# Kernel optimization log

Measured on AMD Instinct MI355X. Metric: run time of the kernel, lower is better.

The kernel has to match this reference:

```python
import jax, jax.numpy as jnp
import numpy as np

N_NODES = 100000


def _graph_conv(x, W, b, src, dst, n_nodes):
    # dgl GraphConv, norm='both'. in_dim >= out_dim so weight is applied first.
    E = src.shape[0]
    ones = jnp.ones((E,), dtype=x.dtype)
    deg_out = jnp.clip(jax.ops.segment_sum(ones, src, num_segments=n_nodes), 1.0)
    deg_in = jnp.clip(jax.ops.segment_sum(ones, dst, num_segments=n_nodes), 1.0)
    h = x @ W                                  # [N, out]
    h = h * (deg_out ** -0.5)[:, None]          # src-side norm D_out^{-1/2}
    agg = jax.ops.segment_sum(h[src], dst, num_segments=n_nodes)  # SpMM
    agg = agg * (deg_in ** -0.5)[:, None]       # dst-side norm D_in^{-1/2}
    return agg + b


def setup_inputs() -> dict:
    key = jax.random.key(0)
    k1, k2, k3, k4, k5, k6, k7 = jax.random.split(key, 7)
    in_dim, hidden_dim, out_dim = 256, 128, 40
    E = 3200000
    h = jax.random.normal(k1, (N_NODES, in_dim), dtype=jnp.float32)
    src = jax.random.randint(k2, (E,), 0, N_NODES)
    dst = jax.random.randint(k3, (E,), 0, N_NODES)
    # Glorot-style init for GraphConv weights, zero bias (dgl default)
    W1 = jax.random.normal(k4, (in_dim, hidden_dim), dtype=jnp.float32) / np.sqrt(in_dim)
    b1 = jnp.zeros((hidden_dim,), dtype=jnp.float32)
    W2 = jax.random.normal(k5, (hidden_dim, out_dim), dtype=jnp.float32) / np.sqrt(hidden_dim)
    b2 = jnp.zeros((out_dim,), dtype=jnp.float32)
    return {"h": h, "W1": W1, "b1": b1, "W2": W2, "b2": b2, "src": src, "dst": dst}


def reference(h, W1, b1, W2, b2, src, dst):
    n = h.shape[0]
    # CRD: GraphConv -> relu (dropout is identity in eval)
    x = _graph_conv(h, W1, b1, src, dst, n)
    x = jax.nn.relu(x)
    # CLS: GraphConv -> log_softmax over classes
    x = _graph_conv(x, W2, b2, src, dst, n)
    return jax.nn.log_softmax(x, axis=1)
```

## Files before the change

kernel.cpp:

```cpp
#include <hip/hip_runtime.h>
#include <hip/hip_bf16.h>
#include <cstddef>
#include <cstdint>

#define IN_DIM 256
#define HID 128
#define OUT_DIM 40

#define CHUNK 8192
#define BIN_SHIFT 10
#define BIN_SIZE 1024
#define MAXB 128
#define GSPLIT 8

typedef __attribute__((ext_vector_type(8))) short short8;
typedef __attribute__((ext_vector_type(4))) float f32x4;
typedef __attribute__((ext_vector_type(2))) float f32x2;

__device__ inline short f2bf(float f) {
    __hip_bfloat16 b = __float2bfloat16(f);
    return __builtin_bit_cast(short, b);
}
__device__ inline float bf2f(unsigned short u) {
    unsigned int v = (unsigned int)u << 16;
    return __builtin_bit_cast(float, v);
}
__device__ inline int permf(int p) { return (p >> 3) + 16 * (p & 7); }

__global__ __launch_bounds__(256) void k_binscatter(const int* __restrict__ src, const int* __restrict__ dst,
                                                    uint32_t* __restrict__ stD, unsigned short* __restrict__ stS,
                                                    int* __restrict__ bboD, int* __restrict__ bboS,
                                                    int E, int NBINS) {
    __shared__ int hD[MAXB], hS[MAXB], cD[MAXB], cS[MAXB], sd[MAXB];
    int j = blockIdx.x, t = threadIdx.x;
    int base = j * CHUNK;
    int nE = min(CHUNK, E - base);
    int NB1 = NBINS + 1;
    for (int i = t; i < MAXB; i += 256) { hD[i] = 0; hS[i] = 0; }
    __syncthreads();
    for (int i = t; i < nE; i += 256) {
        atomicAdd(&hD[dst[base + i] >> BIN_SHIFT], 1);
        atomicAdd(&hS[src[base + i] >> BIN_SHIFT], 1);
    }
    __syncthreads();
    if (t < MAXB) sd[t] = hD[t];
    __syncthreads();
    for (int off = 1; off < MAXB; off <<= 1) {
        int x = 0;
        if (t < MAXB && t >= off) x = sd[t - off];
        __syncthreads();
        if (t < MAXB) sd[t] += x;
        __syncthreads();
    }
    if (t < MAXB) cD[t] = sd[t] - hD[t];
    if (t < NBINS) bboD[(size_t)j * NB1 + t] = sd[t] - hD[t];
    if (t == NBINS) bboD[(size_t)j * NB1 + NBINS] = nE;
    __syncthreads();
    if (t < MAXB) sd[t] = hS[t];
    __syncthreads();
    for (int off = 1; off < MAXB; off <<= 1) {
        int x = 0;
        if (t < MAXB && t >= off) x = sd[t - off];
        __syncthreads();
        if (t < MAXB) sd[t] += x;
        __syncthreads();
    }
    if (t < MAXB) cS[t] = sd[t] - hS[t];
    if (t < NBINS) bboS[(size_t)j * NB1 + t] = sd[t] - hS[t];
    if (t == NBINS) bboS[(size_t)j * NB1 + NBINS] = nE;
    __syncthreads();
    for (int i = t; i < nE; i += 256) {
        int s = src[base + i], d = dst[base + i];
        int pD = atomicAdd(&cD[d >> BIN_SHIFT], 1);
        stD[(size_t)base + pD] = ((uint32_t)(d & (BIN_SIZE - 1)) << 17) | (uint32_t)s;
        int pS = atomicAdd(&cS[s >> BIN_SHIFT], 1);
        stS[(size_t)base + pS] = (unsigned short)(s & (BIN_SIZE - 1));
    }
}

__global__ __launch_bounds__(256) void k_deg_dst(const uint32_t* __restrict__ stD, const int* __restrict__ bboD,
                                                 int* __restrict__ deg_in, int* __restrict__ hsave,
                                                 int N, int nchunk, int NBINS) {
    __shared__ int hist[BIN_SIZE];
    int b = blockIdx.x, g = blockIdx.y, t = threadIdx.x;
    int wv = t >> 6, lane = t & 63;
    int NB1 = NBINS + 1;
    for (int i = t; i < BIN_SIZE; i += 256) hist[i] = 0;
    __syncthreads();
    for (int j = g * 4 + wv; j < nchunk; j += GSPLIT * 4) {
        int s = bboD[(size_t)j * NB1 + b], e = bboD[(size_t)j * NB1 + b + 1];
        const uint32_t* seg = stD + (size_t)j * CHUNK;
        for (int i = s + lane; i < e; i += 64)
            atomicAdd(&hist[seg[i] >> 17], 1);
    }
    __syncthreads();
    int base = b << BIN_SHIFT;
    int* hp = hsave + ((size_t)(b * GSPLIT + g) << BIN_SHIFT);
    for (int i = t; i < BIN_SIZE; i += 256) {
        int v = hist[i];
        hp[i] = v;
        if (v) atomicAdd(&deg_in[base + i], v);
    }
}

__global__ __launch_bounds__(256) void k_deg_src(const unsigned short* __restrict__ stS, const int* __restrict__ bboS,
                                                 int* __restrict__ deg_out, int N, int nchunk, int NBINS) {
    __shared__ int hist[BIN_SIZE];
    int b = blockIdx.x, g = blockIdx.y, t = threadIdx.x;
    int wv = t >> 6, lane = t & 63;
    int NB1 = NBINS + 1;
    for (int i = t; i < BIN_SIZE; i += 256) hist[i] = 0;
    __syncthreads();
    for (int j = g * 4 + wv; j < nchunk; j += GSPLIT * 4) {
        int s = bboS[(size_t)j * NB1 + b], e = bboS[(size_t)j * NB1 + b + 1];
        const unsigned short* seg = stS + (size_t)j * CHUNK;
        for (int i = s + lane; i < e; i += 64)
            atomicAdd(&hist[seg[i]], 1);
    }
    __syncthreads();
    int base = b << BIN_SHIFT;
    for (int i = t; i < BIN_SIZE; i += 256) {
        int v = hist[i];
        if (v) atomicAdd(&deg_out[base + i], v);
    }
}

__global__ __launch_bounds__(256) void k_col(const uint32_t* __restrict__ stD, const int* __restrict__ bboD,
                                             const int* __restrict__ hsave, int* __restrict__ cursor,
                                             int* __restrict__ col, int N, int nchunk, int NBINS) {
    __shared__ int hist[BIN_SIZE];
    int b = blockIdx.x, g = blockIdx.y, t = threadIdx.x;
    int wv = t >> 6, lane = t & 63;
    int NB1 = NBINS + 1;
    int base = b << BIN_SHIFT;
    const int* hp = hsave + ((size_t)(b * GSPLIT + g) << BIN_SHIFT);
    for (int i = t; i < BIN_SIZE; i += 256) {
        int v = hp[i];
        hist[i] = v ? atomicAdd(&cursor[base + i], v) : 0;
    }
    __syncthreads();
    for (int j = g * 4 + wv; j < nchunk; j += GSPLIT * 4) {
        int s = bboD[(size_t)j * NB1 + b], e = bboD[(size_t)j * NB1 + b + 1];
        const uint32_t* seg = stD + (size_t)j * CHUNK;
        for (int i = s + lane; i < e; i += 64) {
            uint32_t v = seg[i];
            int pos = atomicAdd(&hist[v >> 17], 1);
            col[pos] = (int)(v & 0x1FFFFu);
        }
    }
}

__global__ __launch_bounds__(256) void k_scan1(const int* __restrict__ deg, int* __restrict__ out,
                                               int* __restrict__ bsum, float* __restrict__ rs_in, int n) {
    __shared__ int sd[256];
    int t = threadIdx.x, b = blockIdx.x;
    int base = b * 1024 + t * 4;
    int v0 = 0, v1 = 0, v2 = 0, v3 = 0;
    if (base + 0 < n) v0 = deg[base + 0];
    if (base + 1 < n) v1 = deg[base + 1];
    if (base + 2 < n) v2 = deg[base + 2];
    if (base + 3 < n) v3 = deg[base + 3];
    if (base + 0 < n) rs_in[base + 0] = rsqrtf((float)max(v0, 1));
    if (base + 1 < n) rs_in[base + 1] = rsqrtf((float)max(v1, 1));
    if (base + 2 < n) rs_in[base + 2] = rsqrtf((float)max(v2, 1));
    if (base + 3 < n) rs_in[base + 3] = rsqrtf((float)max(v3, 1));
    int ts = v0 + v1 + v2 + v3;
    sd[t] = ts;
    __syncthreads();
    for (int off = 1; off < 256; off <<= 1) {
        int x = 0;
        if (t >= off) x = sd[t - off];
        __syncthreads();
        sd[t] += x;
        __syncthreads();
    }
    int excl = sd[t] - ts;
    if (base + 0 < n) out[base + 0] = excl;
    if (base + 1 < n) out[base + 1] = excl + v0;
    if (base + 2 < n) out[base + 2] = excl + v0 + v1;
    if (base + 3 < n) out[base + 3] = excl + v0 + v1 + v2;
    if (t == 255) bsum[b] = sd[255];
}

__global__ __launch_bounds__(1024) void k_scan2(int* __restrict__ bsum, int nb) {
    __shared__ int sd[1024];
    int t = threadIdx.x;
    int v = (t < nb) ? bsum[t] : 0;
    sd[t] = v;
    __syncthreads();
    for (int off = 1; off < 1024; off <<= 1) {
        int x = 0;
        if (t >= off) x = sd[t - off];
        __syncthreads();
        sd[t] += x;
        __syncthreads();
    }
    if (t < nb) bsum[t] = sd[t] - v;
}

__global__ __launch_bounds__(256) void k_scan3(int* __restrict__ row_ptr, const int* __restrict__ bsum,
                                               int* __restrict__ cursor, const int* __restrict__ deg_out,
                                               float* __restrict__ rs_out, int n, int E) {
    int i = blockIdx.x * 256 + threadIdx.x;
    if (i < n) {
        int v = row_ptr[i] + bsum[i >> 10];
        row_ptr[i] = v;
        cursor[i] = v;
        rs_out[i] = rsqrtf((float)max(deg_out[i], 1));
    }
    if (i == 0) row_ptr[n] = E;
}

__global__ __launch_bounds__(256) void k_wrepack(const float* __restrict__ B, short* __restrict__ Wg) {
    int u = blockIdx.x * 256 + threadIdx.x;
    int k = u >> 5;
    int n0 = (u & 31) * 4;
    float4 v = *(const float4*)(B + (size_t)k * HID + n0);
    int ks = k >> 5, quad = (k >> 3) & 3, j = k & 7;
    float vv[4] = {v.x, v.y, v.z, v.w};
#pragma unroll
    for (int e = 0; e < 4; ++e) {
        int n = n0 + e;
        int nt = n >> 4;
        int ln = (n & 15) | (quad << 4);
        Wg[(((nt * 8 + ks) * 64) + ln) * 8 + j] = f2bf(vv[e]);
    }
}

__global__ __launch_bounds__(256) void k_w2repack(const float* __restrict__ W2, const float* __restrict__ b1,
                                                  short* __restrict__ Wg2, float* __restrict__ b1p) {
    int t = blockIdx.x * 256 + threadIdx.x;
    if (t < 3 * 4 * 64 * 8) {
        int f = t >> 9;
        int ln = (t >> 3) & 63;
        int j = t & 7;
        int nt = f >> 2, ks = f & 3;
        int q = ks * 32 + (ln >> 4) * 8 + j;
        int c = nt * 16 + (ln & 15);
        float v = (c < OUT_DIM) ? W2[(size_t)permf(q) * OUT_DIM + c] : 0.f;
        Wg2[t] = f2bf(v);
    }
    if (t < HID) b1p[t] = b1[permf(t)];
}

__global__ __launch_bounds__(256) void k_gemm1(const float* __restrict__ A, const short* __restrict__ Wg,
                                               const float* __restrict__ rs_out, uint32_t* __restrict__ h1f, int M) {
    __shared__ short As[64 * 264];
    int t = threadIdx.x;
    int lane = t & 63, wv = t >> 6;
    int block_row = blockIdx.x * 64;
#pragma unroll
    for (int i = 0; i < 16; ++i) {
        int u = t + i * 256;
        int row = u >> 6, kq = (u & 63) * 4;
        int gr = block_row + row;
        float4 v = {0.f, 0.f, 0.f, 0.f};
        if (gr < M) v = *(const float4*)(A + (size_t)gr * IN_DIM + kq);
        short4 sv = {f2bf(v.x), f2bf(v.y), f2bf(v.z), f2bf(v.w)};
        *(short4*)&As[row * 264 + kq] = sv;
    }
    __syncthreads();
    f32x4 acc[8] = {};
    int arow = (wv * 16 + (lane & 15)) * 264 + (lane >> 4) * 8;
#pragma unroll
    for (int ks = 0; ks < 8; ++ks) {
        short8 a = *(short8*)&As[arow + ks * 32];
#pragma unroll
        for (int nt = 0; nt < 8; ++nt) {
            short8 b = *(const short8*)&Wg[(((nt * 8 + ks) * 64) + lane) * 8];
            acc[nt] = __builtin_amdgcn_mfma_f32_16x16x32_bf16(a, b, acc[nt], 0, 0, 0);
        }
    }
    int quad = lane >> 4, cl = lane & 15;
#pragma unroll
    for (int r = 0; r < 4; ++r) {
        int gr = block_row + wv * 16 + quad * 4 + r;
        if (gr >= M) continue;
        float sc = rs_out[gr];
        int d0 = __builtin_amdgcn_cvt_pk_fp8_f32(acc[0][r] * sc, acc[1][r] * sc, 0, false);
        d0 = __builtin_amdgcn_cvt_pk_fp8_f32(acc[2][r] * sc, acc[3][r] * sc, d0, true);
        int d1 = __builtin_amdgcn_cvt_pk_fp8_f32(acc[4][r] * sc, acc[5][r] * sc, 0, false);
        d1 = __builtin_amdgcn_cvt_pk_fp8_f32(acc[6][r] * sc, acc[7][r] * sc, d1, true);
        uint2 dd = make_uint2((uint32_t)d0, (uint32_t)d1);
        *(uint2*)((char*)h1f + (size_t)gr * 128 + cl * 8) = dd;
    }
}

__global__ __launch_bounds__(256) void k_spmm1f(const uint2* __restrict__ h1f2, const int* __restrict__ rp,
                                                const int* __restrict__ col, const float* __restrict__ rs_in,
                                                const float* __restrict__ rs_out, const float* __restrict__ b1p,
                                                const short* __restrict__ Wg2,
                                                unsigned char* __restrict__ h2f, int N) {
    __shared__ uint32_t x1s[16 * 64];
    __shared__ uint32_t hs[160];
    int t = threadIdx.x;
    int wv = t >> 6, lane = t & 63;
    int grp = lane >> 4, ql = lane & 15;
    int w_base = blockIdx.x * 16;

    int ntl = (wv < 3) ? wv : 0;
    short8 wf0 = *(const short8*)&Wg2[((ntl * 4 + 0) * 64 + lane) * 8];
    short8 wf1 = *(const short8*)&Wg2[((ntl * 4 + 1) * 64 + lane) * 8];
    short8 wf2 = *(const short8*)&Wg2[((ntl * 4 + 2) * 64 + lane) * 8];
    short8 wf3 = *(const short8*)&Wg2[((ntl * 4 + 3) * 64 + lane) * 8];
    float4 blo = *(const float4*)&b1p[ql * 8];
    float4 bhi = *(const float4*)&b1p[ql * 8 + 4];

    for (int i = t; i < 16 * 64; i += 256) x1s[i] = 0;
    __syncthreads();

#pragma unroll 1
    for (int q = 0; q < 4; ++q) {
        int nloc = wv * 4 + q;
        int w = w_base + nloc;
        if (w < N) {
            int s = rp[w], e = rp[w + 1];
            float acc[8] = {};
            int i = s;
            while (i < e) {
                int cnt = min(64, e - i);
                int cl = (lane < cnt) ? lane : cnt - 1;
                int cidx = col[i + cl];
                for (int it = 0; it < cnt; it += 8) {
                    int eA = it + grp, eB = it + 4 + grp;
                    int cA = __shfl(cidx, eA, 64);
                    int cB = __shfl(cidx, eB, 64);
                    float mA = (eA < cnt) ? 1.f : 0.f;
                    float mB = (eB < cnt) ? 1.f : 0.f;
                    uint2 uA = h1f2[(size_t)cA * 16 + ql];
                    uint2 uB = h1f2[(size_t)cB * 16 + ql];
                    {
                        f32x2 p0 = __builtin_amdgcn_cvt_pk_f32_fp8(uA.x, false);
                        f32x2 p1 = __builtin_amdgcn_cvt_pk_f32_fp8(uA.x, true);
                        f32x2 p2 = __builtin_amdgcn_cvt_pk_f32_fp8(uA.y, false);
                        f32x2 p3 = __builtin_amdgcn_cvt_pk_f32_fp8(uA.y, true);
                        acc[0] = fmaf(p0.x, mA, acc[0]); acc[1] = fmaf(p0.y, mA, acc[1]);
                        acc[2] = fmaf(p1.x, mA, acc[2]); acc[3] = fmaf(p1.y, mA, acc[3]);
                        acc[4] = fmaf(p2.x, mA, acc[4]); acc[5] = fmaf(p2.y, mA, acc[5]);
                        acc[6] = fmaf(p3.x, mA, acc[6]); acc[7] = fmaf(p3.y, mA, acc[7]);
                    }
                    {
                        f32x2 p0 = __builtin_amdgcn_cvt_pk_f32_fp8(uB.x, false);
                        f32x2 p1 = __builtin_amdgcn_cvt_pk_f32_fp8(uB.x, true);
                        f32x2 p2 = __builtin_amdgcn_cvt_pk_f32_fp8(uB.y, false);
                        f32x2 p3 = __builtin_amdgcn_cvt_pk_f32_fp8(uB.y, true);
                        acc[0] = fmaf(p0.x, mB, acc[0]); acc[1] = fmaf(p0.y, mB, acc[1]);
                        acc[2] = fmaf(p1.x, mB, acc[2]); acc[3] = fmaf(p1.y, mB, acc[3]);
                        acc[4] = fmaf(p2.x, mB, acc[4]); acc[5] = fmaf(p2.y, mB, acc[5]);
                        acc[6] = fmaf(p3.x, mB, acc[6]); acc[7] = fmaf(p3.y, mB, acc[7]);
                    }
                }
                i += cnt;
            }
#pragma unroll
            for (int j = 0; j < 8; ++j) {
                acc[j] += __shfl_xor(acc[j], 16, 64);
                acc[j] += __shfl_xor(acc[j], 32, 64);
            }
            if (lane < 16) {
                float sc = rs_in[w];
                float f0, f1;
                uint32_t o0, o1, o2, o3;
                f0 = fmaxf(fmaf(acc[0], sc, blo.x), 0.f); f1 = fmaxf(fmaf(acc[1], sc, blo.y), 0.f);
                o0 = (uint32_t)(unsigned short)f2bf(f0) | ((uint32_t)(unsigned short)f2bf(f1) << 16);
                f0 = fmaxf(fmaf(acc[2], sc, blo.z), 0.f); f1 = fmaxf(fmaf(acc[3], sc, blo.w), 0.f);
                o1 = (uint32_t)(unsigned short)f2bf(f0) | ((uint32_t)(unsigned short)f2bf(f1) << 16);
                f0 = fmaxf(fmaf(acc[4], sc, bhi.x), 0.f); f1 = fmaxf(fmaf(acc[5], sc, bhi.y), 0.f);
                o2 = (uint32_t)(unsigned short)f2bf(f0) | ((uint32_t)(unsigned short)f2bf(f1) << 16);
                f0 = fmaxf(fmaf(acc[6], sc, bhi.z), 0.f); f1 = fmaxf(fmaf(acc[7], sc, bhi.w), 0.f);
                o3 = (uint32_t)(unsigned short)f2bf(f0) | ((uint32_t)(unsigned short)f2bf(f1) << 16);
                int woff = (nloc * 256 + ql * 16) ^ ((nloc & 7) << 4);
                *(uint4*)((char*)x1s + woff) = make_uint4(o0, o1, o2, o3);
            }
        }
    }
    __syncthreads();
    int vr = min(16, N - w_base);
    if (wv < 3) {
        int row = lane & 15, kc = lane >> 4;
        int rbase = row * 256 + kc * 16;
        int swz = (row & 7) << 4;
        f32x4 c = {};
        c = __builtin_amdgcn_mfma_f32_16x16x32_bf16(*(short8*)((char*)x1s + ((rbase + 0) ^ swz)),   wf0, c, 0, 0, 0);
        c = __builtin_amdgcn_mfma_f32_16x16x32_bf16(*(short8*)((char*)x1s + ((rbase + 64) ^ swz)),  wf1, c, 0, 0, 0);
        c = __builtin_amdgcn_mfma_f32_16x16x32_bf16(*(short8*)((char*)x1s + ((rbase + 128) ^ swz)), wf2, c, 0, 0, 0);
        c = __builtin_amdgcn_mfma_f32_16x16x32_bf16(*(short8*)((char*)x1s + ((rbase + 192) ^ swz)), wf3, c, 0, 0, 0);
        int cc = wv * 16 + row;
        int r0 = kc * 4;
        if (cc < OUT_DIM) {
#pragma unroll
            for (int r = 0; r < 4; ++r) {
                int node = r0 + r;
                if (node < vr) {
                    float v = c[r] * rs_out[w_base + node];
                    int pk = __builtin_amdgcn_cvt_pk_fp8_f32(v, v, 0, false);
                    ((unsigned char*)hs)[node * 40 + cc] = (unsigned char)(pk & 0xff);
                }
            }
        }
    }
    __syncthreads();
    uint32_t* dp = (uint32_t*)(h2f + (size_t)w_base * 40);
    for (int idx = t; idx < vr * 10; idx += 256) dp[idx] = hs[idx];
}

__global__ __launch_bounds__(256) void k_spmm2(const unsigned char* __restrict__ h2f, const int* __restrict__ rp,
                                               const int* __restrict__ col, const float* __restrict__ rs_in,
                                               const float* __restrict__ b2, float* __restrict__ out, int n) {
    int w = (blockIdx.x * 256 + threadIdx.x) >> 6;
    int lane = threadIdx.x & 63;
    if (w >= n) return;
    int grp = lane / 5;
    int dw = lane - grp * 5;
    bool gval = grp < 12;
    int s = rp[w], e = rp[w + 1];
    float acc[8] = {};
    int i = s;
    while (i < e) {
        int cnt = min(64, e - i);
        int cl = (lane < cnt) ? lane : cnt - 1;
        int cidx = col[i + cl];
        for (int it = 0; it < cnt; it += 24) {
            int eA = it + grp, eB = it + 12 + grp;
            int cA = __shfl(cidx, eA & 63, 64);
            int cB = __shfl(cidx, eB & 63, 64);
            float mA = (gval && eA < cnt) ? 1.f : 0.f;
            float mB = (gval && eB < cnt) ? 1.f : 0.f;
            uint2 uA = *(const uint2*)(h2f + (size_t)cA * 40 + dw * 8);
            uint2 uB = *(const uint2*)(h2f + (size_t)cB * 40 + dw * 8);
            {
                f32x2 p0 = __builtin_amdgcn_cvt_pk_f32_fp8(uA.x, false);
                f32x2 p1 = __builtin_amdgcn_cvt_pk_f32_fp8(uA.x, true);
                f32x2 p2 = __builtin_amdgcn_cvt_pk_f32_fp8(uA.y, false);
                f32x2 p3 = __builtin_amdgcn_cvt_pk_f32_fp8(uA.y, true);
                acc[0] = fmaf(p0.x, mA, acc[0]); acc[1] = fmaf(p0.y, mA, acc[1]);
                acc[2] = fmaf(p1.x, mA, acc[2]); acc[3] = fmaf(p1.y, mA, acc[3]);
                acc[4] = fmaf(p2.x, mA, acc[4]); acc[5] = fmaf(p2.y, mA, acc[5]);
                acc[6] = fmaf(p3.x, mA, acc[6]); acc[7] = fmaf(p3.y, mA, acc[7]);
            }
            {
                f32x2 p0 = __builtin_amdgcn_cvt_pk_f32_fp8(uB.x, false);
                f32x2 p1 = __builtin_amdgcn_cvt_pk_f32_fp8(uB.x, true);
                f32x2 p2 = __builtin_amdgcn_cvt_pk_f32_fp8(uB.y, false);
                f32x2 p3 = __builtin_amdgcn_cvt_pk_f32_fp8(uB.y, true);
                acc[0] = fmaf(p0.x, mB, acc[0]); acc[1] = fmaf(p0.y, mB, acc[1]);
                acc[2] = fmaf(p1.x, mB, acc[2]); acc[3] = fmaf(p1.y, mB, acc[3]);
                acc[4] = fmaf(p2.x, mB, acc[4]); acc[5] = fmaf(p2.y, mB, acc[5]);
                acc[6] = fmaf(p3.x, mB, acc[6]); acc[7] = fmaf(p3.y, mB, acc[7]);
            }
        }
        i += cnt;
    }
#pragma unroll
    for (int j = 0; j < 8; ++j) {
        acc[j] += __shfl(acc[j], (lane + 30) & 63, 64);
        acc[j] += __shfl(acc[j], (lane + 15) & 63, 64);
        acc[j] += __shfl(acc[j], (lane + 5) & 63, 64) + __shfl(acc[j], (lane + 10) & 63, 64);
    }
    bool act = lane < 5;
    float sc = rs_in[w];
    float val[8];
#pragma unroll
    for (int j = 0; j < 8; ++j)
        val[j] = fmaf(acc[j], sc, b2[dw * 8 + j]);
    float pm = -INFINITY;
    if (act) {
        pm = val[0];
#pragma unroll
        for (int j = 1; j < 8; ++j) pm = fmaxf(pm, val[j]);
    }
    pm = fmaxf(pm, __shfl_xor(pm, 4, 8));
    pm = fmaxf(pm, __shfl_xor(pm, 2, 8));
    pm = fmaxf(pm, __shfl_xor(pm, 1, 8));
    float ex = 0.f;
    if (act) {
#pragma unroll
        for (int j = 0; j < 8; ++j) ex += expf(val[j] - pm);
    }
    ex += __shfl_xor(ex, 4, 8);
    ex += __shfl_xor(ex, 2, 8);
    ex += __shfl_xor(ex, 1, 8);
    if (act) {
        float l = pm + logf(ex);
        float4 o0 = {val[0] - l, val[1] - l, val[2] - l, val[3] - l};
        float4 o1 = {val[4] - l, val[5] - l, val[6] - l, val[7] - l};
        float* op = out + (size_t)w * OUT_DIM + dw * 8;
        *(float4*)op = o0;
        *(float4*)(op + 4) = o1;
    }
}


extern "C" void kernel_launch(void* const* d_in, const int* in_sizes, int n_in,
                              void* d_out, int out_size, void* d_ws, size_t ws_size,
                              hipStream_t stream) {
    const int N = in_sizes[0] / IN_DIM;
    const int E = in_sizes[5];
    const float* h  = (const float*)d_in[0];
    const float* W1 = (const float*)d_in[1];
    const float* b1 = (const float*)d_in[2];
    const float* W2 = (const float*)d_in[3];
    const float* b2 = (const float*)d_in[4];
    const int* src  = (const int*)d_in[5];
    const int* dst  = (const int*)d_in[6];
    float* out = (float*)d_out;

    const int NBINS  = (N + BIN_SIZE - 1) >> BIN_SHIFT;
    const int NCHUNK = (E + CHUNK - 1) / CHUNK;

    char* w = (char*)d_ws;
    size_t off = 0;
    auto alloc = [&](size_t bytes) -> void* {
        void* p = w + off;
        off += (bytes + 255) & ~(size_t)255;
        return p;
    };
    int* deg_in   = (int*)alloc((size_t)N * 4);
    int* deg_out  = (int*)alloc((size_t)N * 4);
    int* row_ptr  = (int*)alloc((size_t)(N + 1) * 4);
    int* cursor   = (int*)alloc((size_t)N * 4);
    int* bsum     = (int*)alloc(1024 * 4);
    float* rs_out = (float*)alloc((size_t)N * 4);
    float* rs_in  = (float*)alloc((size_t)N * 4);
    int* col      = (int*)alloc((size_t)E * 4);
    int* bboD     = (int*)alloc((size_t)NCHUNK * (NBINS + 1) * 4);
    int* bboS     = (int*)alloc((size_t)NCHUNK * (NBINS + 1) * 4);
    short* Wg     = (short*)alloc((size_t)8 * 8 * 64 * 8 * 2);
    short* Wg2    = (short*)alloc((size_t)3 * 4 * 64 * 8 * 2);
    float* b1p    = (float*)alloc((size_t)HID * 4);
    int* hsave    = (int*)alloc((size_t)NBINS * GSPLIT * BIN_SIZE * 4);
    size_t stD_bytes = (size_t)E * 4;  if ((size_t)N * HID > stD_bytes) stD_bytes = (size_t)N * HID;
    size_t stS_bytes = (size_t)E * 2;  if ((size_t)N * OUT_DIM > stS_bytes) stS_bytes = (size_t)N * OUT_DIM;
    uint32_t* stD = (uint32_t*)alloc(stD_bytes);
    unsigned short* stS = (unsigned short*)alloc(stS_bytes);
    uint32_t* h1f = (uint32_t*)stD;
    unsigned char* h2f = (unsigned char*)stS;

    int gN = (N + 255) / 256;
    int NB = (N + 1023) / 1024;

    hipMemsetAsync(deg_in, 0, (size_t)N * 4, stream);
    hipMemsetAsync(deg_out, 0, (size_t)N * 4, stream);
    k_wrepack<<<32, 256, 0, stream>>>(W1, Wg);
    k_w2repack<<<24, 256, 0, stream>>>(W2, b1, Wg2, b1p);
    k_binscatter<<<NCHUNK, 256, 0, stream>>>(src, dst, stD, stS, bboD, bboS, E, NBINS);
    k_deg_src<<<dim3(NBINS, GSPLIT), 256, 0, stream>>>(stS, bboS, deg_out, N, NCHUNK, NBINS);
    k_deg_dst<<<dim3(NBINS, GSPLIT), 256, 0, stream>>>(stD, bboD, deg_in, hsave, N, NCHUNK, NBINS);
    k_scan1<<<NB, 256, 0, stream>>>(deg_in, row_ptr, bsum, rs_in, N);
    k_scan2<<<1, 1024, 0, stream>>>(bsum, NB);
    k_scan3<<<gN, 256, 0, stream>>>(row_ptr, bsum, cursor, deg_out, rs_out, N, E);
    k_col<<<dim3(NBINS, GSPLIT), 256, 0, stream>>>(stD, bboD, hsave, cursor, col, N, NCHUNK, NBINS);
    k_gemm1<<<(N + 63) / 64, 256, 0, stream>>>(h, Wg, rs_out, h1f, N);
    k_spmm1f<<<(N + 15) / 16, 256, 0, stream>>>((const uint2*)h1f, row_ptr, col, rs_in, rs_out, b1p, Wg2, h2f, N);
    k_spmm2<<<(N + 3) / 4, 256, 0, stream>>>(h2f, row_ptr, col, rs_in, b2, out, N);
}
```

Baseline: 485.2 us.

## Pad layer-2 features to 64B rows, shrink spmm1f blocks, merge setup and degree kernels

Pads the fp8 layer-2 feature rows from 40 to 64 bytes so the second SpMM gathers aligned 8-byte chunks with 8 lanes per edge and reduces with xor shuffles. The fused SpMM1+GEMM2 kernel now handles 4 nodes per block, one per wave, instead of 16, raising block count and dropping the per-wave node loop. Weight repacking and degree zeroing move into one setup kernel, and the two degree-histogram kernels merge into one launch, cutting launch overhead. In exchange, the MFMA in spmm1f runs on mostly empty rows, and layer-2 feature storage and gather traffic grow.

Measured after the change: 467.4 us. -3.7%, faster.

```diff
diff --git a/kernel.cpp b/kernel.cpp
--- a/kernel.cpp
+++ b/kernel.cpp
@@ -26,6 +26,46 @@
     return __builtin_bit_cast(float, v);
 }
 __device__ inline int permf(int p) { return (p >> 3) + 16 * (p & 7); }
+
+__global__ __launch_bounds__(256) void k_setup(const float* __restrict__ W1, const float* __restrict__ W2,
+                                               const float* __restrict__ b1, short* __restrict__ Wg,
+                                               short* __restrict__ Wg2, float* __restrict__ b1p,
+                                               int* __restrict__ deg_in, int* __restrict__ deg_out, int Z) {
+    int flat = blockIdx.x * 256 + threadIdx.x;
+    if (flat < 8192) {
+        int k = flat >> 5;
+        int n0 = (flat & 31) * 4;
+        float4 v = *(const float4*)(W1 + (size_t)k * HID + n0);
+        int ks = k >> 5, quad = (k >> 3) & 3, j = k & 7;
+        float vv[4] = {v.x, v.y, v.z, v.w};
+#pragma unroll
+        for (int e = 0; e < 4; ++e) {
+            int n = n0 + e;
+            int nt = n >> 4;
+            int ln = (n & 15) | (quad << 4);
+            Wg[(((nt * 8 + ks) * 64) + ln) * 8 + j] = f2bf(vv[e]);
+        }
+        return;
+    }
+    flat -= 8192;
+    if (flat < 3 * 4 * 64 * 8) {
+        int f = flat >> 9;
+        int ln = (flat >> 3) & 63;
+        int j = flat & 7;
+        int nt = f >> 2, ks = f & 3;
+        int q = ks * 32 + (ln >> 4) * 8 + j;
+        int c = nt * 16 + (ln & 15);
+        float v = (c < OUT_DIM) ? W2[(size_t)permf(q) * OUT_DIM + c] : 0.f;
+        Wg2[flat] = f2bf(v);
+        return;
+    }
+    flat -= 3 * 4 * 64 * 8;
+    if (flat < HID) { b1p[flat] = b1[permf(flat)]; return; }
+    flat -= HID;
+    if (flat < Z) { *(int4*)(deg_in + flat * 4) = make_int4(0, 0, 0, 0); return; }
+    flat -= Z;
+    if (flat < Z) { *(int4*)(deg_out + flat * 4) = make_int4(0, 0, 0, 0); }
+}
 
 __global__ __launch_bounds__(256) void k_binscatter(const int* __restrict__ src, const int* __restrict__ dst,
                                                     uint32_t* __restrict__ stD, unsigned short* __restrict__ stS,
@@ -78,50 +118,43 @@
     }
 }
 
-__global__ __launch_bounds__(256) void k_deg_dst(const uint32_t* __restrict__ stD, const int* __restrict__ bboD,
-                                                 int* __restrict__ deg_in, int* __restrict__ hsave,
-                                                 int N, int nchunk, int NBINS) {
+__global__ __launch_bounds__(256) void k_deg(const uint32_t* __restrict__ stD, const int* __restrict__ bboD,
+                                             const unsigned short* __restrict__ stS, const int* __restrict__ bboS,
+                                             int* __restrict__ deg_in, int* __restrict__ deg_out,
+                                             int* __restrict__ hsave, int nchunk, int NBINS) {
     __shared__ int hist[BIN_SIZE];
     int b = blockIdx.x, g = blockIdx.y, t = threadIdx.x;
     int wv = t >> 6, lane = t & 63;
     int NB1 = NBINS + 1;
     for (int i = t; i < BIN_SIZE; i += 256) hist[i] = 0;
     __syncthreads();
-    for (int j = g * 4 + wv; j < nchunk; j += GSPLIT * 4) {
-        int s = bboD[(size_t)j * NB1 + b], e = bboD[(size_t)j * NB1 + b + 1];
-        const uint32_t* seg = stD + (size_t)j * CHUNK;
-        for (int i = s + lane; i < e; i += 64)
-            atomicAdd(&hist[seg[i] >> 17], 1);
-    }
-    __syncthreads();
     int base = b << BIN_SHIFT;
-    int* hp = hsave + ((size_t)(b * GSPLIT + g) << BIN_SHIFT);
-    for (int i = t; i < BIN_SIZE; i += 256) {
-        int v = hist[i];
-        hp[i] = v;
-        if (v) atomicAdd(&deg_in[base + i], v);
-    }
-}
-
-__global__ __launch_bounds__(256) void k_deg_src(const unsigned short* __restrict__ stS, const int* __restrict__ bboS,
-                                                 int* __restrict__ deg_out, int N, int nchunk, int NBINS) {
-    __shared__ int hist[BIN_SIZE];
-    int b = blockIdx.x, g = blockIdx.y, t = threadIdx.x;
-    int wv = t >> 6, lane = t & 63;
-    int NB1 = NBINS + 1;
-    for (int i = t; i < BIN_SIZE; i += 256) hist[i] = 0;
-    __syncthreads();
-    for (int j = g * 4 + wv; j < nchunk; j += GSPLIT * 4) {
-        int s = bboS[(size_t)j * NB1 + b], e = bboS[(size_t)j * NB1 + b + 1];
-        const unsigned short* seg = stS + (size_t)j * CHUNK;
-        for (int i = s + lane; i < e; i += 64)
-            atomicAdd(&hist[seg[i]], 1);
-    }
-    __syncthreads();
-    int base = b << BIN_SHIFT;
-    for (int i = t; i < BIN_SIZE; i += 256) {
-        int v = hist[i];
-        if (v) atomicAdd(&deg_out[base + i], v);
+    if (blockIdx.z == 0) {
+        for (int j = g * 4 + wv; j < nchunk; j += GSPLIT * 4) {
+            int s = bboD[(size_t)j * NB1 + b], e = bboD[(size_t)j * NB1 + b + 1];
+            const uint32_t* seg = stD + (size_t)j * CHUNK;
+            for (int i = s + lane; i < e; i += 64)
+                atomicAdd(&hist[seg[i] >> 17], 1);
+        }
+        __syncthreads();
+        int* hp = hsave + ((size_t)(b * GSPLIT + g) << BIN_SHIFT);
+        for (int i = t; i < BIN_SIZE; i += 256) {
+            int v = hist[i];
+            hp[i] = v;
+            if (v) atomicAdd(&deg_in[base + i], v);
+        }
+    } else {
+        for (int j = g * 4 + wv; j < nchunk; j += GSPLIT * 4) {
+            int s = bboS[(size_t)j * NB1 + b], e = bboS[(size_t)j * NB1 + b + 1];
+            const unsigned short* seg = stS + (size_t)j * CHUNK;
+            for (int i = s + lane; i < e; i += 64)
+                atomicAdd(&hist[seg[i]], 1);
+        }
+        __syncthreads();
+        for (int i = t; i < BIN_SIZE; i += 256) {
+            int v = hist[i];
+            if (v) atomicAdd(&deg_out[base + i], v);
+        }
     }
 }
 
@@ -211,38 +244,6 @@
     if (i == 0) row_ptr[n] = E;
 }
 
-__global__ __launch_bounds__(256) void k_wrepack(const float* __restrict__ B, short* __restrict__ Wg) {
-    int u = blockIdx.x * 256 + threadIdx.x;
-    int k = u >> 5;
-    int n0 = (u & 31) * 4;
-    float4 v = *(const float4*)(B + (size_t)k * HID + n0);
-    int ks = k >> 5, quad = (k >> 3) & 3, j = k & 7;
-    float vv[4] = {v.x, v.y, v.z, v.w};
-#pragma unroll
-    for (int e = 0; e < 4; ++e) {
-        int n = n0 + e;
-        int nt = n >> 4;
-        int ln = (n & 15) | (quad << 4);
-        Wg[(((nt * 8 + ks) * 64) + ln) * 8 + j] = f2bf(vv[e]);
-    }
-}
-
-__global__ __launch_bounds__(256) void k_w2repack(const float* __restrict__ W2, const float* __restrict__ b1,
-                                                  short* __restrict__ Wg2, float* __restrict__ b1p) {
-    int t = blockIdx.x * 256 + threadIdx.x;
-    if (t < 3 * 4 * 64 * 8) {
-        int f = t >> 9;
-        int ln = (t >> 3) & 63;
-        int j = t & 7;
-        int nt = f >> 2, ks = f & 3;
-        int q = ks * 32 + (ln >> 4) * 8 + j;
-        int c = nt * 16 + (ln & 15);
-        float v = (c < OUT_DIM) ? W2[(size_t)permf(q) * OUT_DIM + c] : 0.f;
-        Wg2[t] = f2bf(v);
-    }
-    if (t < HID) b1p[t] = b1[permf(t)];
-}
-
 __global__ __launch_bounds__(256) void k_gemm1(const float* __restrict__ A, const short* __restrict__ Wg,
                                                const float* __restrict__ rs_out, uint32_t* __restrict__ h1f, int M) {
     __shared__ short As[64 * 264];
@@ -290,13 +291,14 @@
                                                 const int* __restrict__ col, const float* __restrict__ rs_in,
                                                 const float* __restrict__ rs_out, const float* __restrict__ b1p,
                                                 const short* __restrict__ Wg2,
-                                                unsigned char* __restrict__ h2f, int N) {
+                                                uint32_t* __restrict__ h2f, int N) {
     __shared__ uint32_t x1s[16 * 64];
-    __shared__ uint32_t hs[160];
+    __shared__ uint32_t hs[4 * 16];
     int t = threadIdx.x;
     int wv = t >> 6, lane = t & 63;
     int grp = lane >> 4, ql = lane & 15;
-    int w_base = blockIdx.x * 16;
+    int w_base = blockIdx.x * 4;
+    int w = w_base + wv;
 
     int ntl = (wv < 3) ? wv : 0;
     short8 wf0 = *(const short8*)&Wg2[((ntl * 4 + 0) * 64 + lane) * 8];
@@ -305,77 +307,70 @@
     short8 wf3 = *(const short8*)&Wg2[((ntl * 4 + 3) * 64 + lane) * 8];
     float4 blo = *(const float4*)&b1p[ql * 8];
     float4 bhi = *(const float4*)&b1p[ql * 8 + 4];
-
-    for (int i = t; i < 16 * 64; i += 256) x1s[i] = 0;
-    __syncthreads();
-
-#pragma unroll 1
-    for (int q = 0; q < 4; ++q) {
-        int nloc = wv * 4 + q;
-        int w = w_base + nloc;
-        if (w < N) {
-            int s = rp[w], e = rp[w + 1];
-            float acc[8] = {};
-            int i = s;
-            while (i < e) {
-                int cnt = min(64, e - i);
-                int cl = (lane < cnt) ? lane : cnt - 1;
-                int cidx = col[i + cl];
-                for (int it = 0; it < cnt; it += 8) {
-                    int eA = it + grp, eB = it + 4 + grp;
-                    int cA = __shfl(cidx, eA, 64);
-                    int cB = __shfl(cidx, eB, 64);
-                    float mA = (eA < cnt) ? 1.f : 0.f;
-                    float mB = (eB < cnt) ? 1.f : 0.f;
-                    uint2 uA = h1f2[(size_t)cA * 16 + ql];
-                    uint2 uB = h1f2[(size_t)cB * 16 + ql];
-                    {
-                        f32x2 p0 = __builtin_amdgcn_cvt_pk_f32_fp8(uA.x, false);
-                        f32x2 p1 = __builtin_amdgcn_cvt_pk_f32_fp8(uA.x, true);
-                        f32x2 p2 = __builtin_amdgcn_cvt_pk_f32_fp8(uA.y, false);
-                        f32x2 p3 = __builtin_amdgcn_cvt_pk_f32_fp8(uA.y, true);
-                        acc[0] = fmaf(p0.x, mA, acc[0]); acc[1] = fmaf(p0.y, mA, acc[1]);
-                        acc[2] = fmaf(p1.x, mA, acc[2]); acc[3] = fmaf(p1.y, mA, acc[3]);
-                        acc[4] = fmaf(p2.x, mA, acc[4]); acc[5] = fmaf(p2.y, mA, acc[5]);
-                        acc[6] = fmaf(p3.x, mA, acc[6]); acc[7] = fmaf(p3.y, mA, acc[7]);
-                    }
-                    {
-                        f32x2 p0 = __builtin_amdgcn_cvt_pk_f32_fp8(uB.x, false);
-                        f32x2 p1 = __builtin_amdgcn_cvt_pk_f32_fp8(uB.x, true);
-                        f32x2 p2 = __builtin_amdgcn_cvt_pk_f32_fp8(uB.y, false);
-                        f32x2 p3 = __builtin_amdgcn_cvt_pk_f32_fp8(uB.y, true);
-                        acc[0] = fmaf(p0.x, mB, acc[0]); acc[1] = fmaf(p0.y, mB, acc[1]);
-                        acc[2] = fmaf(p1.x, mB, acc[2]); acc[3] = fmaf(p1.y, mB, acc[3]);
-                        acc[4] = fmaf(p2.x, mB, acc[4]); acc[5] = fmaf(p2.y, mB, acc[5]);
-                        acc[6] = fmaf(p3.x, mB, acc[6]); acc[7] = fmaf(p3.y, mB, acc[7]);
-                    }
+    if (t < 24) hs[(t / 6) * 16 + 10 + (t % 6)] = 0;
+
+    if (w < N) {
+        int s = rp[w], e = rp[w + 1];
+        float acc[8] = {};
+        int i = s;
+        while (i < e) {
+            int cnt = min(64, e - i);
+            int cl = (lane < cnt) ? lane : cnt - 1;
+            int cidx = col[i + cl];
+            for (int it = 0; it < cnt; it += 8) {
+                int eA = it + grp, eB = it + 4 + grp;
+                int cA = __shfl(cidx, eA, 64);
+                int cB = __shfl(cidx, eB, 64);
+                float mA = (eA < cnt) ? 1.f : 0.f;
+                float mB = (eB < cnt) ? 1.f : 0.f;
+                uint2 uA = h1f2[(size_t)cA * 16 + ql];
+                uint2 uB = h1f2[(size_t)cB * 16 + ql];
+                {
+                    f32x2 p0 = __builtin_amdgcn_cvt_pk_f32_fp8(uA.x, false);
+                    f32x2 p1 = __builtin_amdgcn_cvt_pk_f32_fp8(uA.x, true);
+                    f32x2 p2 = __builtin_amdgcn_cvt_pk_f32_fp8(uA.y, false);
+                    f32x2 p3 = __builtin_amdgcn_cvt_pk_f32_fp8(uA.y, true);
+                    acc[0] = fmaf(p0.x, mA, acc[0]); acc[1] = fmaf(p0.y, mA, acc[1]);
+                    acc[2] = fmaf(p1.x, mA, acc[2]); acc[3] = fmaf(p1.y, mA, acc[3]);
+                    acc[4] = fmaf(p2.x, mA, acc[4]); acc[5] = fmaf(p2.y, mA, acc[5]);
+                    acc[6] = fmaf(p3.x, mA, acc[6]); acc[7] = fmaf(p3.y, mA, acc[7]);
                 }
-                i += cnt;
+                {
+                    f32x2 p0 = __builtin_amdgcn_cvt_pk_f32_fp8(uB.x, false);
+                    f32x2 p1 = __builtin_amdgcn_cvt_pk_f32_fp8(uB.x, true);
+                    f32x2 p2 = __builtin_amdgcn_cvt_pk_f32_fp8(uB.y, false);
+                    f32x2 p3 = __builtin_amdgcn_cvt_pk_f32_fp8(uB.y, true);
+                    acc[0] = fmaf(p0.x, mB, acc[0]); acc[1] = fmaf(p0.y, mB, acc[1]);
+                    acc[2] = fmaf(p1.x, mB, acc[2]); acc[3] = fmaf(p1.y, mB, acc[3]);
+                    acc[4] = fmaf(p2.x, mB, acc[4]); acc[5] = fmaf(p2.y, mB, acc[5]);
+                    acc[6] = fmaf(p3.x, mB, acc[6]); acc[7] = fmaf(p3.y, mB, acc[7]);
+                }
             }
-#pragma unroll
-            for (int j = 0; j < 8; ++j) {
-                acc[j] += __shfl_xor(acc[j], 16, 64);
-                acc[j] += __shfl_xor(acc[j], 32, 64);
-            }
-            if (lane < 16) {
-                float sc = rs_in[w];
-                float f0, f1;
-                uint32_t o0, o1, o2, o3;
-                f0 = fmaxf(fmaf(acc[0], sc, blo.x), 0.f); f1 = fmaxf(fmaf(acc[1], sc, blo.y), 0.f);
-                o0 = (uint32_t)(unsigned short)f2bf(f0) | ((uint32_t)(unsigned short)f2bf(f1) << 16);
-                f0 = fmaxf(fmaf(acc[2], sc, blo.z), 0.f); f1 = fmaxf(fmaf(acc[3], sc, blo.w), 0.f);
-                o1 = (uint32_t)(unsigned short)f2bf(f0) | ((uint32_t)(unsigned short)f2bf(f1) << 16);
-                f0 = fmaxf(fmaf(acc[4], sc, bhi.x), 0.f); f1 = fmaxf(fmaf(acc[5], sc, bhi.y), 0.f);
-                o2 = (uint32_t)(unsigned short)f2bf(f0) | ((uint32_t)(unsigned short)f2bf(f1) << 16);
-                f0 = fmaxf(fmaf(acc[6], sc, bhi.z), 0.f); f1 = fmaxf(fmaf(acc[7], sc, bhi.w), 0.f);
-                o3 = (uint32_t)(unsigned short)f2bf(f0) | ((uint32_t)(unsigned short)f2bf(f1) << 16);
-                int woff = (nloc * 256 + ql * 16) ^ ((nloc & 7) << 4);
-                *(uint4*)((char*)x1s + woff) = make_uint4(o0, o1, o2, o3);
-            }
-        }
-    }
-    __syncthreads();
-    int vr = min(16, N - w_base);
+            i += cnt;
+        }
+#pragma unroll
+        for (int j = 0; j < 8; ++j) {
+            acc[j] += __shfl_xor(acc[j], 16, 64);
+            acc[j] += __shfl_xor(acc[j], 32, 64);
+        }
+        if (lane < 16) {
+            float sc = rs_in[w];
+            float f0, f1;
+            uint32_t o0, o1, o2, o3;
+            f0 = fmaxf(fmaf(acc[0], sc, blo.x), 0.f); f1 = fmaxf(fmaf(acc[1], sc, blo.y), 0.f);
+            o0 = (uint32_t)(unsigned short)f2bf(f0) | ((uint32_t)(unsigned short)f2bf(f1) << 16);
+            f0 = fmaxf(fmaf(acc[2], sc, blo.z), 0.f); f1 = fmaxf(fmaf(acc[3], sc, blo.w), 0.f);
+            o1 = (uint32_t)(unsigned short)f2bf(f0) | ((uint32_t)(unsigned short)f2bf(f1) << 16);
+            f0 = fmaxf(fmaf(acc[4], sc, bhi.x), 0.f); f1 = fmaxf(fmaf(acc[5], sc, bhi.y), 0.f);
+            o2 = (uint32_t)(unsigned short)f2bf(f0) | ((uint32_t)(unsigned short)f2bf(f1) << 16);
+            f0 = fmaxf(fmaf(acc[6], sc, bhi.z), 0.f); f1 = fmaxf(fmaf(acc[7], sc, bhi.w), 0.f);
+            o3 = (uint32_t)(unsigned short)f2bf(f0) | ((uint32_t)(unsigned short)f2bf(f1) << 16);
+            int woff = (wv * 256 + ql * 16) ^ ((wv & 7) << 4);
+            *(uint4*)((char*)x1s + woff) = make_uint4(o0, o1, o2, o3);
+        }
+    }
+    __syncthreads();
+    int vr = min(4, N - w_base);
     if (wv < 3) {
         int row = lane & 15, kc = lane >> 4;
         int rbase = row * 256 + kc * 16;
@@ -386,33 +381,29 @@
         c = __builtin_amdgcn_mfma_f32_16x16x32_bf16(*(short8*)((char*)x1s + ((rbase + 128) ^ swz)), wf2, c, 0, 0, 0);
         c = __builtin_amdgcn_mfma_f32_16x16x32_bf16(*(short8*)((char*)x1s + ((rbase + 192) ^ swz)), wf3, c, 0, 0, 0);
         int cc = wv * 16 + row;
-        int r0 = kc * 4;
-        if (cc < OUT_DIM) {
+        if (cc < OUT_DIM && kc == 0) {
 #pragma unroll
             for (int r = 0; r < 4; ++r) {
-                int node = r0 + r;
-                if (node < vr) {
-                    float v = c[r] * rs_out[w_base + node];
+                if (r < vr) {
+                    float v = c[r] * rs_out[w_base + r];
                     int pk = __builtin_amdgcn_cvt_pk_fp8_f32(v, v, 0, false);
-                    ((unsigned char*)hs)[node * 40 + cc] = (unsigned char)(pk & 0xff);
+                    ((unsigned char*)hs)[r * 64 + cc] = (unsigned char)(pk & 0xff);
                 }
             }
         }
     }
     __syncthreads();
-    uint32_t* dp = (uint32_t*)(h2f + (size_t)w_base * 40);
-    for (int idx = t; idx < vr * 10; idx += 256) dp[idx] = hs[idx];
-}
-
-__global__ __launch_bounds__(256) void k_spmm2(const unsigned char* __restrict__ h2f, const int* __restrict__ rp,
+    uint32_t* dp = h2f + (size_t)w_base * 16;
+    for (int idx = t; idx < vr * 16; idx += 256) dp[idx] = hs[idx];
+}
+
+__global__ __launch_bounds__(256) void k_spmm2(const uint2* __restrict__ h2f2, const int* __restrict__ rp,
                                                const int* __restrict__ col, const float* __restrict__ rs_in,
                                                const float* __restrict__ b2, float* __restrict__ out, int n) {
     int w = (blockIdx.x * 256 + threadIdx.x) >> 6;
     int lane = threadIdx.x & 63;
     if (w >= n) return;
-    int grp = lane / 5;
-    int dw = lane - grp * 5;
-    bool gval = grp < 12;
+    int grp = lane >> 3, fl = lane & 7;
     int s = rp[w], e = rp[w + 1];
     float acc[8] = {};
     int i = s;
@@ -420,14 +411,14 @@
         int cnt = min(64, e - i);
         int cl = (lane < cnt) ? lane : cnt - 1;
         int cidx = col[i + cl];
-        for (int it = 0; it < cnt; it += 24) {
-            int eA = it + grp, eB = it + 12 + grp;
-            int cA = __shfl(cidx, eA & 63, 64);
-            int cB = __shfl(cidx, eB & 63, 64);
-            float mA = (gval && eA < cnt) ? 1.f : 0.f;
-            float mB = (gval && eB < cnt) ? 1.f : 0.f;
-            uint2 uA = *(const uint2*)(h2f + (size_t)cA * 40 + dw * 8);
-            uint2 uB = *(const uint2*)(h2f + (size_t)cB * 40 + dw * 8);
+        for (int it = 0; it < cnt; it += 16) {
+            int eA = it + grp, eB = it + 8 + grp;
+            int cA = __shfl(cidx, eA, 64);
+            int cB = __shfl(cidx, eB, 64);
+            float mA = (eA < cnt) ? 1.f : 0.f;
+            float mB = (eB < cnt) ? 1.f : 0.f;
+            uint2 uA = h2f2[(size_t)cA * 8 + fl];
+            uint2 uB = h2f2[(size_t)cB * 8 + fl];
             {
                 f32x2 p0 = __builtin_amdgcn_cvt_pk_f32_fp8(uA.x, false);
                 f32x2 p1 = __builtin_amdgcn_cvt_pk_f32_fp8(uA.x, true);
@@ -453,16 +444,17 @@
     }
 #pragma unroll
     for (int j = 0; j < 8; ++j) {
-        acc[j] += __shfl(acc[j], (lane + 30) & 63, 64);
-        acc[j] += __shfl(acc[j], (lane + 15) & 63, 64);
-        acc[j] += __shfl(acc[j], (lane + 5) & 63, 64) + __shfl(acc[j], (lane + 10) & 63, 64);
+        acc[j] += __shfl_xor(acc[j], 8, 64);
+        acc[j] += __shfl_xor(acc[j], 16, 64);
+        acc[j] += __shfl_xor(acc[j], 32, 64);
     }
     bool act = lane < 5;
     float sc = rs_in[w];
+    int bb = (fl < 5) ? fl * 8 : 0;
     float val[8];
 #pragma unroll
     for (int j = 0; j < 8; ++j)
-        val[j] = fmaf(acc[j], sc, b2[dw * 8 + j]);
+        val[j] = fmaf(acc[j], sc, b2[bb + j]);
     float pm = -INFINITY;
     if (act) {
         pm = val[0];
@@ -484,7 +476,7 @@
         float l = pm + logf(ex);
         float4 o0 = {val[0] - l, val[1] - l, val[2] - l, val[3] - l};
         float4 o1 = {val[4] - l, val[5] - l, val[6] - l, val[7] - l};
-        float* op = out + (size_t)w * OUT_DIM + dw * 8;
+        float* op = out + (size_t)w * OUT_DIM + lane * 8;
         *(float4*)op = o0;
         *(float4*)(op + 4) = o1;
     }
@@ -530,27 +522,26 @@
     float* b1p    = (float*)alloc((size_t)HID * 4);
     int* hsave    = (int*)alloc((size_t)NBINS * GSPLIT * BIN_SIZE * 4);
     size_t stD_bytes = (size_t)E * 4;  if ((size_t)N * HID > stD_bytes) stD_bytes = (size_t)N * HID;
-    size_t stS_bytes = (size_t)E * 2;  if ((size_t)N * OUT_DIM > stS_bytes) stS_bytes = (size_t)N * OUT_DIM;
+    size_t stS_bytes = (size_t)E * 2;  if ((size_t)N * 64 > stS_bytes) stS_bytes = (size_t)N * 64;
     uint32_t* stD = (uint32_t*)alloc(stD_bytes);
     unsigned short* stS = (unsigned short*)alloc(stS_bytes);
     uint32_t* h1f = (uint32_t*)stD;
-    unsigned char* h2f = (unsigned char*)stS;
+    uint32_t* h2f = (uint32_t*)stS;
 
     int gN = (N + 255) / 256;
     int NB = (N + 1023) / 1024;
-
-    hipMemsetAsync(deg_in, 0, (size_t)N * 4, stream);
-    hipMemsetAsync(deg_out, 0, (size_t)N * 4, stream);
-    k_wrepack<<<32, 256, 0, stream>>>(W1, Wg);
-    k_w2repack<<<24, 256, 0, stream>>>(W2, b1, Wg2, b1p);
+    int Z = (N + 3) / 4;
+    int setup_units = 8192 + 3 * 4 * 64 * 8 + HID + 2 * Z;
+    int gsetup = (setup_units + 255) / 256;
+
+    k_setup<<<gsetup, 256, 0, stream>>>(W1, W2, b1, Wg, Wg2, b1p, deg_in, deg_out, Z);
     k_binscatter<<<NCHUNK, 256, 0, stream>>>(src, dst, stD, stS, bboD, bboS, E, NBINS);
-    k_deg_src<<<dim3(NBINS, GSPLIT), 256, 0, stream>>>(stS, bboS, deg_out, N, NCHUNK, NBINS);
-    k_deg_dst<<<dim3(NBINS, GSPLIT), 256, 0, stream>>>(stD, bboD, deg_in, hsave, N, NCHUNK, NBINS);
+    k_deg<<<dim3(NBINS, GSPLIT, 2), 256, 0, stream>>>(stD, bboD, stS, bboS, deg_in, deg_out, hsave, NCHUNK, NBINS);
     k_scan1<<<NB, 256, 0, stream>>>(deg_in, row_ptr, bsum, rs_in, N);
     k_scan2<<<1, 1024, 0, stream>>>(bsum, NB);
     k_scan3<<<gN, 256, 0, stream>>>(row_ptr, bsum, cursor, deg_out, rs_out, N, E);
     k_col<<<dim3(NBINS, GSPLIT), 256, 0, stream>>>(stD, bboD, hsave, cursor, col, N, NCHUNK, NBINS);
     k_gemm1<<<(N + 63) / 64, 256, 0, stream>>>(h, Wg, rs_out, h1f, N);
-    k_spmm1f<<<(N + 15) / 16, 256, 0, stream>>>((const uint2*)h1f, row_ptr, col, rs_in, rs_out, b1p, Wg2, h2f, N);
-    k_spmm2<<<(N + 3) / 4, 256, 0, stream>>>(h2f, row_ptr, col, rs_in, b2, out, N);
-}
+    k_spmm1f<<<(N + 3) / 4, 256, 0, stream>>>((const uint2*)h1f, row_ptr, col, rs_in, rs_out, b1p, Wg2, h2f, N);
+    k_spmm2<<<(N + 3) / 4, 256, 0, stream>>>((const uint2*)h2f, row_ptr, col, rs_in, b2, out, N);
+}
```
